# Optimization experiments

Hardware: AMD Instinct MI355X
Metric: run time of the kernel (lower is better)

Reference implementation:

```python
import jax, jax.numpy as jnp
import numpy as np

B = 65536
N_HOSTS = 16
N_FEATS = 48        # 3 * n_hosts
N_WINDOW = 3
N_LATENT = 10
GAT_IN = 3
GAT_OUT = 16
E = N_WINDOW + GAT_OUT  # 19, MHA embed dim
PROTO_DIM = 10


def setup_inputs() -> dict:
    key = jax.random.key(0)
    ks = jax.random.split(key, 20)
    def rn(k, shape, scale=0.1):
        return jax.random.normal(k, shape, dtype=jnp.float32) * scale
    return {
        "t": jax.random.normal(ks[0], (B, N_WINDOW, N_FEATS), dtype=jnp.float32),
        "s": jnp.zeros((1,), jnp.float32),  # unused by forward, kept for signature fidelity
        "h0": jax.random.normal(ks[1], (B, 1, N_WINDOW), dtype=jnp.float32),
        "gru_Wih": rn(ks[2], (3 * N_WINDOW, N_FEATS)),
        "gru_Whh": rn(ks[3], (3 * N_WINDOW, N_WINDOW)),
        "gru_bih": rn(ks[4], (3 * N_WINDOW,)),
        "gru_bhh": rn(ks[5], (3 * N_WINDOW,)),
        "gat_W": rn(ks[6], (GAT_IN, GAT_OUT)),
        "gat_al": rn(ks[7], (GAT_OUT,)),
        "gat_ar": rn(ks[8], (GAT_OUT,)),
        "mha_Win": rn(ks[9], (3 * E, E)),
        "mha_bin": rn(ks[10], (3 * E,)),
        "mha_Wout": rn(ks[11], (E, E)),
        "mha_bout": rn(ks[12], (E,)),
        "enc_W": rn(ks[13], (N_HOSTS * N_LATENT, N_WINDOW * E)),
        "enc_b": rn(ks[14], (N_HOSTS * N_LATENT,)),
        "anom_W": rn(ks[15], (2, N_LATENT)),
        "anom_b": rn(ks[16], (2,)),
        "proto_W": rn(ks[17], (PROTO_DIM, N_LATENT)),
        "proto_b": rn(ks[18], (PROTO_DIM,)),
    }


def _forward(t, s, h0, gru_Wih, gru_Whh, gru_bih, gru_bhh,
             gat_W, gat_al, gat_ar, mha_Win, mha_bin, mha_Wout, mha_bout,
             enc_W, enc_b, anom_W, anom_b, proto_W, proto_b):
    # ---- GRU (seq-first, batch B, hidden = n_window = 3) ----
    xs = jnp.swapaxes(t, 0, 1)  # (3, B, 48)
    h0_ = h0[:, 0, :]           # (B, 3)

    def gru_step(h, x_t):
        gi = x_t @ gru_Wih.T + gru_bih   # (B, 9)
        gh = h @ gru_Whh.T + gru_bhh     # (B, 9)
        i_r, i_z, i_n = jnp.split(gi, 3, axis=-1)
        h_r, h_z, h_n = jnp.split(gh, 3, axis=-1)
        r = jax.nn.sigmoid(i_r + h_r)
        z = jax.nn.sigmoid(i_z + h_z)
        n = jnp.tanh(i_n + r * h_n)
        h_new = (1.0 - z) * n + z * h
        return h_new, h_new

    _, gru_out = jax.lax.scan(gru_step, h0_, xs)  # (3, B, 3)

    # ---- GAT on fully-connected 16-node graph (with self loops) ----
    gin = t.reshape(t.shape[0], N_WINDOW, N_HOSTS, GAT_IN)      # (B, 3, 16, 3)
    z = jnp.einsum("bwnc,cf->bwnf", gin, gat_W)                 # (B, 3, 16, 16)
    el = z @ gat_al                                              # src scores (B,3,16)
    er = z @ gat_ar                                              # dst scores (B,3,16)
    e = jax.nn.leaky_relu(er[..., :, None] + el[..., None, :], 0.2)  # (B,3,v,u)
    alpha = jax.nn.softmax(e, axis=-1)                           # softmax over sources u
    gat_nodes = jnp.einsum("bwvu,bwuf->bwvf", alpha, z)          # (B, 3, 16, 16)
    gat_out = gat_nodes.mean(axis=2)                             # (B, 3, 16) mean over hosts
    gat_out = jnp.swapaxes(gat_out, 0, 1)                        # (3, B, 16)

    # ---- concat + single-head MHA (embed=19) ----
    c = jnp.concatenate([gru_out, gat_out], axis=-1)             # (3, B, 19)
    Wq, Wk, Wv = jnp.split(mha_Win, 3, axis=0)
    bq, bk, bv = jnp.split(mha_bin, 3, axis=0)
    q = c @ Wq.T + bq
    k = c @ Wk.T + bk
    v = c @ Wv.T + bv
    scores = jnp.einsum("sbe,tbe->bst", q, k) / jnp.sqrt(jnp.float32(E))
    attw = jax.nn.softmax(scores, axis=-1)
    attn = jnp.einsum("bst,tbe->sbe", attw, v)
    attn = attn @ mha_Wout.T + mha_bout                          # (3, B, 19)

    # ---- encoder: Linear(57,160); LeakyReLU(True) => negative_slope=1.0 => identity ----
    flat = jnp.swapaxes(attn, 0, 1).reshape(-1, N_WINDOW * E)    # (B, 57), seq-major flatten
    latent = flat @ enc_W.T + enc_b                              # (B, 160)
    latent = latent.reshape(-1, N_HOSTS, N_LATENT)               # (B, 16, 10)

    # ---- per-host tiny decoders, vectorized ----
    anomaly = jax.nn.softmax(latent @ anom_W.T + anom_b, axis=-1)   # (B, 16, 2)
    proto = jax.nn.sigmoid(latent @ proto_W.T + proto_b)            # (B, 16, PROTO_DIM)
    return anomaly, proto


def reference(t, s, h0, gru_Wih, gru_Whh, gru_bih, gru_bhh,
              gat_W, gat_al, gat_ar, mha_Win, mha_bin, mha_Wout, mha_bout,
              enc_W, enc_b, anom_W, anom_b, proto_W, proto_b):
    return _forward(t, s, h0, gru_Wih, gru_Whh, gru_bih, gru_bhh,
                    gat_W, gat_al, gat_ar, mha_Win, mha_bin, mha_Wout, mha_bout,
                    enc_W, enc_b, anom_W, anom_b, proto_W, proto_b)
```

## Files before the change

kernel.cpp:

```cpp
#include <hip/hip_runtime.h>

#define NW 3
#define NF 48
#define NHOST 16
#define NLAT 10
#define GOUT 16
#define EDIM 19
#define PDIM 10

#define CB_M    0
#define CB_P    361
#define CB_G    722
#define CB_H    741
#define CB_R    760
#define CB_C0   779
#define CB_WAL  780
#define CB_WAR  783
#define CB_CBIG 800
#define CB_BF   976
#define CB_TOT  10240

typedef __attribute__((ext_vector_type(8))) short bf16x8;
typedef __attribute__((ext_vector_type(4))) float f32x4;

__device__ __forceinline__ float frcp(float x){ return __builtin_amdgcn_rcpf(x); }
__device__ __forceinline__ float fsig(float x){ return frcp(1.f + __expf(-x)); }
__device__ __forceinline__ float ftanh(float x){ return 1.f - 2.f*frcp(1.f + __expf(2.f*x)); }
__device__ __forceinline__ unsigned short f2bf(float x){
    union { float f; unsigned u; } v; v.f = x;
    unsigned r = v.u + 0x7FFFu + ((v.u >> 16) & 1u);
    return (unsigned short)(r >> 16);
}

__global__ __launch_bounds__(256) void k_const(
    const float* __restrict__ Win, const float* __restrict__ bin,
    const float* __restrict__ Wout, const float* __restrict__ bout,
    const float* __restrict__ gatW, const float* __restrict__ gal,
    const float* __restrict__ gar, const float* __restrict__ encW,
    const float* __restrict__ encb,
    const float* __restrict__ aW, const float* __restrict__ ab,
    const float* __restrict__ pW, const float* __restrict__ pb,
    float* __restrict__ cb)
{
    const int w = blockIdx.x*blockDim.x + threadIdx.x;
    if (w < 786) {
        const int idx = w;
        float acc = 0.f;
        if (idx < 361) {
            int i = idx/19, j = idx%19;
            for (int e = 0; e < EDIM; ++e) acc += Win[e*EDIM+i]*Win[(EDIM+e)*EDIM+j];
        } else if (idx < 722) {
            int k = idx-361; int i = k/19, j = k%19;
            for (int e = 0; e < EDIM; ++e) acc += Wout[i*EDIM+e]*Win[(2*EDIM+e)*EDIM+j];
        } else if (idx < 741) {
            int j = idx-722;
            for (int e = 0; e < EDIM; ++e) acc += bin[e]*Win[(EDIM+e)*EDIM+j];
        } else if (idx < 760) {
            int i = idx-741;
            for (int e = 0; e < EDIM; ++e) acc += Win[e*EDIM+i]*bin[EDIM+e];
        } else if (idx < 779) {
            int i = idx-760; acc = bout[i];
            for (int e = 0; e < EDIM; ++e) acc += Wout[i*EDIM+e]*bin[2*EDIM+e];
        } else if (idx == 779) {
            for (int e = 0; e < EDIM; ++e) acc += bin[e]*bin[EDIM+e];
        } else {
            int c = idx-780; int cc = c%3; bool left = c<3;
            for (int f2 = 0; f2 < GOUT; ++f2)
                acc += gatW[cc*GOUT+f2]*(left ? gal[f2] : gar[f2]);
        }
        cb[idx] = acc;
    } else if (w < 962) {
        const int g = w - 786;
        int host = g / 11, jj = g % 11;
        float acc = (jj == 0) ? (ab[0] - ab[1]) : pb[jj-1];
        for (int l = 0; l < NLAT; ++l) {
            float coef = (jj == 0) ? (aW[l] - aW[NLAT+l]) : pW[(jj-1)*NLAT + l];
            acc += coef * encb[host*NLAT + l];
        }
        cb[CB_CBIG + g] = acc;
    } else if (w < 12226) {
        unsigned short* bf = (unsigned short*)(cb + CB_BF);
        const int u = w - 962;
        int j    = u & 7;
        int lane = (u >> 3) & 63;
        int tile = u >> 9;
        int half = tile / 11, n = tile % 11;
        int k = half*32 + ((lane >> 4) & 3)*8 + j;
        int g = n*16 + (lane & 15);
        float acc = 0.f;
        if (k < 57) {
            int host = g / 11, jj = g % 11;
            for (int l = 0; l < NLAT; ++l) {
                float coef = (jj == 0) ? (aW[l] - aW[NLAT+l]) : pW[(jj-1)*NLAT + l];
                acc += coef * encW[(host*NLAT + l)*57 + k];
            }
        }
        bf[u] = f2bf(acc);
    }
}

__global__ __launch_bounds__(256) void k_front(
    const float* __restrict__ t, const float* __restrict__ Wih, const float* __restrict__ bih,
    const float* __restrict__ gatW, const float* __restrict__ cb,
    float* __restrict__ ws1, int B)
{
    const int b = blockIdx.x*blockDim.x + threadIdx.x;
    const int w = blockIdx.y;
    if (b >= B) return;

    float x[NF];
    const float* tp = t + ((size_t)b*NW + w)*NF;
#pragma unroll
    for (int i = 0; i < NF/4; ++i) {
        float4 v = *reinterpret_cast<const float4*>(tp + i*4);
        x[i*4+0]=v.x; x[i*4+1]=v.y; x[i*4+2]=v.z; x[i*4+3]=v.w;
    }
    float* o = ws1 + (size_t)w*25*B + b;
#pragma unroll
    for (int r = 0; r < 9; ++r) {
        float acc = bih[r];
#pragma unroll
        for (int j = 0; j < NF; ++j) acc += x[j]*Wih[r*NF+j];
        o[(size_t)r*B] = acc;
    }
    const float Wal0=cb[CB_WAL],Wal1=cb[CB_WAL+1],Wal2=cb[CB_WAL+2];
    const float War0=cb[CB_WAR],War1=cb[CB_WAR+1],War2=cb[CB_WAR+2];
    float el[NHOST], er[NHOST];
#pragma unroll
    for (int n = 0; n < NHOST; ++n) {
        el[n] = x[n*3+0]*Wal0 + x[n*3+1]*Wal1 + x[n*3+2]*Wal2;
        er[n] = x[n*3+0]*War0 + x[n*3+1]*War1 + x[n*3+2]*War2;
    }
    float beta[NHOST];
#pragma unroll
    for (int u = 0; u < NHOST; ++u) beta[u] = 0.f;
#pragma unroll
    for (int v = 0; v < NHOST; ++v) {
        float ee[NHOST]; float sum = 0.f;
#pragma unroll
        for (int u = 0; u < NHOST; ++u) {
            float s = er[v] + el[u];
            s = fmaxf(s, 0.2f*s);
            ee[u] = __expf(s); sum += ee[u];
        }
        float inv = frcp(sum);
#pragma unroll
        for (int u = 0; u < NHOST; ++u) beta[u] += ee[u]*inv;
    }
    float g0=0.f, g1=0.f, g2=0.f;
#pragma unroll
    for (int u = 0; u < NHOST; ++u) {
        float bu = beta[u]*(1.f/16.f);
        g0 += bu*x[u*3+0]; g1 += bu*x[u*3+1]; g2 += bu*x[u*3+2];
    }
#pragma unroll
    for (int f2 = 0; f2 < GOUT; ++f2)
        o[(size_t)(9+f2)*B] = g0*gatW[f2] + g1*gatW[GOUT+f2] + g2*gatW[2*GOUT+f2];
}

__global__ __attribute__((amdgpu_flat_work_group_size(256,256), amdgpu_waves_per_eu(1,1)))
void k_mid(const float* __restrict__ ws1, const float* __restrict__ h0,
           const float* __restrict__ Whh, const float* __restrict__ bhh,
           const float* __restrict__ cb, unsigned short* __restrict__ ws2bf, int B)
{
    const int b = blockIdx.x*blockDim.x + threadIdx.x;
    if (b >= B) return;

    float h[3] = { h0[b*3+0], h0[b*3+1], h0[b*3+2] };
    float cw[NW][EDIM];
#pragma unroll
    for (int w = 0; w < NW; ++w) {
        const float* i1 = ws1 + (size_t)w*25*B + b;
        float gi[9];
#pragma unroll
        for (int r = 0; r < 9; ++r) gi[r] = i1[(size_t)r*B];
        float gh[9];
#pragma unroll
        for (int r = 0; r < 9; ++r)
            gh[r] = bhh[r] + h[0]*Whh[r*3+0] + h[1]*Whh[r*3+1] + h[2]*Whh[r*3+2];
#pragma unroll
        for (int j = 0; j < 3; ++j) {
            float rg = fsig(gi[j]   + gh[j]);
            float zg = fsig(gi[3+j] + gh[3+j]);
            float ng = ftanh(gi[6+j] + rg*gh[6+j]);
            h[j] = (1.f - zg)*ng + zg*h[j];
        }
        cw[w][0]=h[0]; cw[w][1]=h[1]; cw[w][2]=h[2];
#pragma unroll
        for (int f2 = 0; f2 < GOUT; ++f2) cw[w][3+f2] = i1[(size_t)(9+f2)*B];
    }
    float hs[NW];
#pragma unroll
    for (int s = 0; s < NW; ++s) {
        float a = 0.f;
#pragma unroll
        for (int i = 0; i < EDIM; ++i) a += cw[s][i]*cb[CB_H+i];
        hs[s] = a;
    }
    const float c0 = cb[CB_C0];
    float sc[NW][NW];
#pragma unroll
    for (int tt = 0; tt < NW; ++tt) {
        float mt[EDIM];
#pragma unroll
        for (int i = 0; i < EDIM; ++i) {
            float a = 0.f;
#pragma unroll
            for (int j = 0; j < EDIM; ++j) a += cb[CB_M+i*EDIM+j]*cw[tt][j];
            mt[i] = a;
        }
        float gt = 0.f;
#pragma unroll
        for (int j = 0; j < EDIM; ++j) gt += cb[CB_G+j]*cw[tt][j];
#pragma unroll
        for (int s = 0; s < NW; ++s) {
            float a = 0.f;
#pragma unroll
            for (int i = 0; i < EDIM; ++i) a += cw[s][i]*mt[i];
            sc[s][tt] = (a + gt + hs[s] + c0) * 0.2294157338705618f;
        }
    }
    float attw[NW][NW];
#pragma unroll
    for (int s = 0; s < NW; ++s) {
        float m = fmaxf(sc[s][0], fmaxf(sc[s][1], sc[s][2]));
        float e0=__expf(sc[s][0]-m), e1=__expf(sc[s][1]-m), e2=__expf(sc[s][2]-m);
        float inv = frcp(e0+e1+e2);
        attw[s][0]=e0*inv; attw[s][1]=e1*inv; attw[s][2]=e2*inv;
    }
    float fac[NW][EDIM];
#pragma unroll
    for (int s = 0; s < NW; ++s)
#pragma unroll
        for (int i = 0; i < EDIM; ++i) fac[s][i] = cb[CB_R+i];
#pragma unroll
    for (int tt = 0; tt < NW; ++tt) {
        float pc[EDIM];
#pragma unroll
        for (int i = 0; i < EDIM; ++i) {
            float a = 0.f;
#pragma unroll
            for (int j = 0; j < EDIM; ++j) a += cb[CB_P+i*EDIM+j]*cw[tt][j];
            pc[i] = a;
        }
#pragma unroll
        for (int s = 0; s < NW; ++s)
#pragma unroll
            for (int i = 0; i < EDIM; ++i) fac[s][i] += attw[s][tt]*pc[i];
    }
#pragma unroll
    for (int s = 0; s < NW; ++s)
#pragma unroll
        for (int i = 0; i < EDIM; ++i)
            ws2bf[(size_t)(s*EDIM+i)*B + b] = f2bf(fac[s][i]);
#pragma unroll
    for (int r = 57; r < 64; ++r) ws2bf[(size_t)r*B + b] = 0;
}

__global__ __launch_bounds__(256) void k_enc(
    const unsigned short* __restrict__ ws2bf, const float* __restrict__ cb,
    float* __restrict__ outA, float* __restrict__ outP, int B)
{
    __shared__ float lg[64][178];
    const int lane = threadIdx.x & 63;
    const int wv   = __builtin_amdgcn_readfirstlane(threadIdx.x >> 6);
    const int b0   = blockIdx.x*64;
    if (b0 >= B) return;

    const int brow = b0 + wv*16 + (lane & 15);
    const int koff = (lane >> 4) * 8;
    union { bf16x8 v; unsigned short s[8]; } a0, a1;
#pragma unroll
    for (int j = 0; j < 8; ++j) {
        a0.s[j] = ws2bf[(size_t)(koff + j)*B + brow];
        a1.s[j] = ws2bf[(size_t)(32 + koff + j)*B + brow];
    }

    const uint4* bfq = (const uint4*)(cb + CB_BF);
    const int r0 = wv*16 + ((lane >> 4) << 2);
#pragma unroll
    for (int n = 0; n < 11; ++n) {
        union { uint4 q; bf16x8 v; } bf0, bf1;
        bf0.q = bfq[(size_t)n*64 + lane];
        bf1.q = bfq[(size_t)(11 + n)*64 + lane];
        f32x4 acc = {0.f, 0.f, 0.f, 0.f};
        acc = __builtin_amdgcn_mfma_f32_16x16x32_bf16(a0.v, bf0.v, acc, 0, 0, 0);
        acc = __builtin_amdgcn_mfma_f32_16x16x32_bf16(a1.v, bf1.v, acc, 0, 0, 0);
        const int c = n*16 + (lane & 15);
#pragma unroll
        for (int r = 0; r < 4; ++r) lg[r0 + r][c] = acc[r];
    }
    __syncthreads();

    const int host = threadIdx.x & 15;
    const int tg   = threadIdx.x >> 4;
    const float* cbig = cb + CB_CBIG;
#pragma unroll
    for (int i = 0; i < 4; ++i) {
        const int bl = tg + 16*i;
        const int b  = b0 + bl;
        float v[11];
#pragma unroll
        for (int jj = 0; jj < 11; ++jj)
            v[jj] = lg[bl][host*11 + jj] + cbig[host*11 + jj];
        float p0 = fsig(v[0]);
        float2 av; av.x = p0; av.y = 1.f - p0;
        *reinterpret_cast<float2*>(outA + (size_t)b*32 + host*2) = av;
        float* pP = outP + (size_t)b*160 + host*10;
#pragma unroll
        for (int p = 0; p < 5; ++p) {
            float2 pv; pv.x = fsig(v[1 + 2*p]); pv.y = fsig(v[2 + 2*p]);
            *reinterpret_cast<float2*>(pP + 2*p) = pv;
        }
    }
}

extern "C" void kernel_launch(void* const* d_in, const int* in_sizes, int n_in,
                              void* d_out, int out_size, void* d_ws, size_t ws_size,
                              hipStream_t stream) {
    const float* t    = (const float*)d_in[0];
    const float* h0   = (const float*)d_in[2];
    const float* Wih  = (const float*)d_in[3];
    const float* Whh  = (const float*)d_in[4];
    const float* bih  = (const float*)d_in[5];
    const float* bhh  = (const float*)d_in[6];
    const float* gatW = (const float*)d_in[7];
    const float* gal  = (const float*)d_in[8];
    const float* gar  = (const float*)d_in[9];
    const float* Win  = (const float*)d_in[10];
    const float* bin  = (const float*)d_in[11];
    const float* Wout = (const float*)d_in[12];
    const float* bout = (const float*)d_in[13];
    const float* encW = (const float*)d_in[14];
    const float* encb = (const float*)d_in[15];
    const float* aW   = (const float*)d_in[16];
    const float* ab   = (const float*)d_in[17];
    const float* pW   = (const float*)d_in[18];
    const float* pb   = (const float*)d_in[19];

    const int B = in_sizes[0] / (NW * NF);
    float* cb  = (float*)d_ws;
    float* ws1 = cb + CB_TOT;
    unsigned short* ws2bf = (unsigned short*)(ws1 + (size_t)25*NW*B);
    float* outA = (float*)d_out;
    float* outP = (float*)d_out + (size_t)B*32;

    k_const<<<dim3(48), 256, 0, stream>>>(Win, bin, Wout, bout, gatW, gal, gar,
                                          encW, encb, aW, ab, pW, pb, cb);
    k_front<<<dim3((B+255)/256, NW), 256, 0, stream>>>(t, Wih, bih, gatW, cb, ws1, B);
    k_mid<<<dim3((B+255)/256), 256, 0, stream>>>(ws1, h0, Whh, bhh, cb, ws2bf, B);
    k_enc<<<dim3((B+63)/64), 256, 0, stream>>>(ws2bf, cb, outA, outP, B);
}
```

Measured before the change: 77.30 us.

## Store intermediate bf16 activations row-major for vectorized MFMA operand loads

The intermediate bf16 buffer between the mid and encoder kernels moves from a feature-major layout [64][B] to a row-major [B][64] layout. The mid kernel now writes each row as eight 16-byte packed stores, and the encoder kernel loads its MFMA A fragments with two 16-byte loads instead of sixteen strided 2-byte loads. The mid kernel also computes the attention output directly at store time by reusing the cw registers, dropping the separate fac array. In exchange, the mid kernel's per-thread stores are 128-byte strided across lanes rather than coalesced across the batch.

```diff
diff --git a/kernel.cpp b/kernel.cpp
--- a/kernel.cpp
+++ b/kernel.cpp
@@ -167,7 +167,7 @@
     if (b >= B) return;
 
     float h[3] = { h0[b*3+0], h0[b*3+1], h0[b*3+2] };
-    float cw[NW][EDIM];
+    float cw[57];
 #pragma unroll
     for (int w = 0; w < NW; ++w) {
         const float* i1 = ws1 + (size_t)w*25*B + b;
@@ -185,16 +185,16 @@
             float ng = ftanh(gi[6+j] + rg*gh[6+j]);
             h[j] = (1.f - zg)*ng + zg*h[j];
         }
-        cw[w][0]=h[0]; cw[w][1]=h[1]; cw[w][2]=h[2];
-#pragma unroll
-        for (int f2 = 0; f2 < GOUT; ++f2) cw[w][3+f2] = i1[(size_t)(9+f2)*B];
+        cw[w*EDIM+0]=h[0]; cw[w*EDIM+1]=h[1]; cw[w*EDIM+2]=h[2];
+#pragma unroll
+        for (int f2 = 0; f2 < GOUT; ++f2) cw[w*EDIM+3+f2] = i1[(size_t)(9+f2)*B];
     }
     float hs[NW];
 #pragma unroll
     for (int s = 0; s < NW; ++s) {
         float a = 0.f;
 #pragma unroll
-        for (int i = 0; i < EDIM; ++i) a += cw[s][i]*cb[CB_H+i];
+        for (int i = 0; i < EDIM; ++i) a += cw[s*EDIM+i]*cb[CB_H+i];
         hs[s] = a;
     }
     const float c0 = cb[CB_C0];
@@ -206,17 +206,17 @@
         for (int i = 0; i < EDIM; ++i) {
             float a = 0.f;
 #pragma unroll
-            for (int j = 0; j < EDIM; ++j) a += cb[CB_M+i*EDIM+j]*cw[tt][j];
+            for (int j = 0; j < EDIM; ++j) a += cb[CB_M+i*EDIM+j]*cw[tt*EDIM+j];
             mt[i] = a;
         }
         float gt = 0.f;
 #pragma unroll
-        for (int j = 0; j < EDIM; ++j) gt += cb[CB_G+j]*cw[tt][j];
+        for (int j = 0; j < EDIM; ++j) gt += cb[CB_G+j]*cw[tt*EDIM+j];
 #pragma unroll
         for (int s = 0; s < NW; ++s) {
             float a = 0.f;
 #pragma unroll
-            for (int i = 0; i < EDIM; ++i) a += cw[s][i]*mt[i];
+            for (int i = 0; i < EDIM; ++i) a += cw[s*EDIM+i]*mt[i];
             sc[s][tt] = (a + gt + hs[s] + c0) * 0.2294157338705618f;
         }
     }
@@ -228,11 +228,6 @@
         float inv = frcp(e0+e1+e2);
         attw[s][0]=e0*inv; attw[s][1]=e1*inv; attw[s][2]=e2*inv;
     }
-    float fac[NW][EDIM];
-#pragma unroll
-    for (int s = 0; s < NW; ++s)
-#pragma unroll
-        for (int i = 0; i < EDIM; ++i) fac[s][i] = cb[CB_R+i];
 #pragma unroll
     for (int tt = 0; tt < NW; ++tt) {
         float pc[EDIM];
@@ -240,21 +235,29 @@
         for (int i = 0; i < EDIM; ++i) {
             float a = 0.f;
 #pragma unroll
-            for (int j = 0; j < EDIM; ++j) a += cb[CB_P+i*EDIM+j]*cw[tt][j];
+            for (int j = 0; j < EDIM; ++j) a += cb[CB_P+i*EDIM+j]*cw[tt*EDIM+j];
             pc[i] = a;
         }
 #pragma unroll
-        for (int s = 0; s < NW; ++s)
-#pragma unroll
-            for (int i = 0; i < EDIM; ++i) fac[s][i] += attw[s][tt]*pc[i];
-    }
-#pragma unroll
-    for (int s = 0; s < NW; ++s)
-#pragma unroll
-        for (int i = 0; i < EDIM; ++i)
-            ws2bf[(size_t)(s*EDIM+i)*B + b] = f2bf(fac[s][i]);
-#pragma unroll
-    for (int r = 57; r < 64; ++r) ws2bf[(size_t)r*B + b] = 0;
+        for (int i = 0; i < EDIM; ++i) cw[tt*EDIM+i] = pc[i];
+    }
+    unsigned short* ob = ws2bf + (size_t)b*64;
+#pragma unroll
+    for (int c = 0; c < 8; ++c) {
+        union { uint4 q; unsigned short s[8]; } pk;
+#pragma unroll
+        for (int e = 0; e < 8; ++e) {
+            const int idx = c*8 + e;
+            float val = 0.f;
+            if (idx < 57) {
+                const int s2 = idx / EDIM, i = idx % EDIM;
+                val = cb[CB_R+i] + attw[s2][0]*cw[i] + attw[s2][1]*cw[EDIM+i]
+                    + attw[s2][2]*cw[2*EDIM+i];
+            }
+            pk.s[e] = f2bf(val);
+        }
+        *reinterpret_cast<uint4*>(ob + c*8) = pk.q;
+    }
 }
 
 __global__ __launch_bounds__(256) void k_enc(
@@ -269,12 +272,10 @@
 
     const int brow = b0 + wv*16 + (lane & 15);
     const int koff = (lane >> 4) * 8;
-    union { bf16x8 v; unsigned short s[8]; } a0, a1;
-#pragma unroll
-    for (int j = 0; j < 8; ++j) {
-        a0.s[j] = ws2bf[(size_t)(koff + j)*B + brow];
-        a1.s[j] = ws2bf[(size_t)(32 + koff + j)*B + brow];
-    }
+    const unsigned short* ap = ws2bf + (size_t)brow*64;
+    union { uint4 q; bf16x8 v; } a0, a1;
+    a0.q = *reinterpret_cast<const uint4*>(ap + koff);
+    a1.q = *reinterpret_cast<const uint4*>(ap + 32 + koff);
 
     const uint4* bfq = (const uint4*)(cb + CB_BF);
     const int r0 = wv*16 + ((lane >> 4) << 2);
```

Result: no change. 77.23 us (-0.1%).
